# Optimization experiments

Hardware: AMD Instinct MI355X
Metric: run time of the kernel (lower is better)

The kernel has to match this reference:

```python
import jax, jax.numpy as jnp
import numpy as np

B, N, C, H = 8, 1025, 512, 8
G = 32  # grid size; S = G*G = N-1


def setup_inputs() -> dict:
    key = jax.random.key(0)
    ks = jax.random.split(key, 5)
    return {
        "x": jax.random.normal(ks[0], (B, N, C), dtype=jnp.float32),
        "qkv_w": jax.random.normal(ks[1], (3 * C, C), dtype=jnp.float32) * (C ** -0.5),
        "proj_w": jax.random.normal(ks[2], (C, C), dtype=jnp.float32) * (C ** -0.5),
        "proj_b": jnp.zeros((C,), dtype=jnp.float32),
        "wg_w": jax.random.normal(ks[3], (H, 64), dtype=jnp.float32) * 0.125,
        "wg_b": jnp.zeros((H,), dtype=jnp.float32),
    }


def _geometry_bias(wg_w, wg_b):
    # BoxRelationalEmbedding on a fixed 32x32 grid; batch-independent, so computed once.
    S = G * G
    xs = jnp.arange(G, dtype=jnp.float32)
    px = jnp.repeat(xs, G)   # px_min: row index per flattened cell
    py = jnp.tile(xs, G)     # py_min: col index per flattened cell
    rx0, ry0 = px / G, py / G
    rx1, ry1 = (px + 1.0) / G, (py + 1.0) / G
    cx = 0.5 * (rx0 + rx1)
    cy = 0.5 * (ry0 + ry1)
    w = rx1 - rx0 + 1.0
    h = ry1 - ry0 + 1.0
    dx = jnp.log(jnp.clip(jnp.abs((cx[:, None] - cx[None, :]) / w[:, None]), 1e-3, None))
    dy = jnp.log(jnp.clip(jnp.abs((cy[:, None] - cy[None, :]) / h[:, None]), 1e-3, None))
    dw = jnp.log(w[:, None] / w[None, :])
    dh = jnp.log(h[:, None] / h[None, :])
    pos = jnp.stack([dx, dy, dw, dh], axis=-1)  # [S,S,4]
    dim_mat = 1.0 / jnp.power(1000.0, jnp.arange(8, dtype=jnp.float32) / 8.0)  # dim_g/8 = 8 freqs
    mul = (100.0 * pos)[..., None] * dim_mat        # [S,S,4,8]
    mul = mul.reshape(S, S, 32)
    emb = jnp.concatenate([jnp.sin(mul), jnp.cos(mul)], axis=-1)  # [S,S,64]
    rgw = jax.nn.relu(jnp.einsum('ijd,hd->hij', emb, wg_w) + wg_b[:, None, None])  # [H,S,S]
    rgw = jnp.log(jnp.clip(rgw, 1e-6, None))
    # pad zero column (dim 3 cat of t1) then zero row (dim 2 cat of t2) -> [H, S+1, S+1]
    return jnp.pad(rgw, ((0, 0), (1, 0), (1, 0)))


def reference(x, qkv_w, proj_w, proj_b, wg_w, wg_b):
    b, n, c = x.shape
    hd = c // H
    scale = hd ** -0.5
    bias = _geometry_bias(wg_w, wg_b)  # [H, n, n]
    qkv = (x @ qkv_w.T).reshape(b, n, 3, H, hd)
    q, k, v = qkv[:, :, 0], qkv[:, :, 1], qkv[:, :, 2]  # each [b,n,H,hd]
    attn = jnp.einsum('bihd,bjhd->bhij', q, k) * scale + bias[None]
    attn = jax.nn.softmax(attn, axis=-1)
    out = jnp.einsum('bhij,bjhd->bihd', attn, v).reshape(b, n, c)
    return out @ proj_w.T + proj_b
```

## Files before the change

### kernel.cpp

```cpp
#include <hip/hip_runtime.h>
#include <hip/hip_bf16.h>
#include <math.h>

#define B_  8
#define N_  1025
#define C_  512
#define H_  8
#define HD_ 64
#define M_  (B_ * N_)
#define VCS 2048
#define VST 36

typedef __attribute__((ext_vector_type(8))) short short8;
typedef __attribute__((ext_vector_type(4))) float f32x4;

__device__ inline unsigned short bf16u(float x) {
    __hip_bfloat16 t = __float2bfloat16(x);
    return *(unsigned short*)&t;
}
__device__ inline void load_lds16(const void* g, void* l) {
    __builtin_amdgcn_global_load_lds(
        (const __attribute__((address_space(1))) unsigned int*)g,
        (__attribute__((address_space(3))) unsigned int*)l, 16, 0, 0);
}

#define PER_ ((size_t)B_ * H_ * N_ * HD_)
#define SZ_QKVW (3 * C_ * C_)
#define SZ_PRJW (C_ * C_)
#define CAST_BLKS ((4198400 + 786432 + 262144) / 4 / 256)

__global__ void prep_kernel(const float* __restrict__ x,
                            const float* __restrict__ qkv_w,
                            const float* __restrict__ proj_w,
                            const float* __restrict__ wg_w,
                            const float* __restrict__ wg_b,
                            unsigned short* __restrict__ xb,
                            unsigned short* __restrict__ wqkvb,
                            unsigned short* __restrict__ wprjb,
                            float* __restrict__ tab) {
    int blk = blockIdx.x;
    int tid = threadIdx.x;
    if (blk < 32) {
        int idx = blk * 256 + tid;
        int h = idx >> 10;
        int a = (idx >> 5) & 31;
        int b = idx & 31;
        float dx = logf(fmaxf((float)a * (1.0f / 33.0f), 0.001f));
        float dy = logf(fmaxf((float)b * (1.0f / 33.0f), 0.001f));
        const float* w = wg_w + h * 64;
        float acc = wg_b[h];
#pragma unroll
        for (int k = 0; k < 8; k++) {
            float f = powf(1000.0f, -(float)k * 0.125f);
            float X = 100.0f * dx * f;
            float Y = 100.0f * dy * f;
            acc += w[k]      * sinf(X);
            acc += w[8 + k]  * sinf(Y);
            acc += w[32 + k] * cosf(X);
            acc += w[40 + k] * cosf(Y);
            acc += w[48 + k] + w[56 + k];
        }
        tab[idx] = logf(fmaxf(fmaxf(acc, 0.0f), 1e-6f));
        return;
    }
    long i4 = ((long)(blk - 32) * 256 + tid) * 4;
    const float* src;
    unsigned short* dst;
    long off;
    if (i4 < (long)PER_)                    { src = x;      dst = xb;    off = i4; }
    else if (i4 < (long)PER_ + SZ_QKVW)     { src = qkv_w;  dst = wqkvb; off = i4 - PER_; }
    else                                    { src = proj_w; dst = wprjb; off = i4 - PER_ - SZ_QKVW; }
    float4 v = *(const float4*)(src + off);
    ushort4 p;
    p.x = bf16u(v.x); p.y = bf16u(v.y); p.z = bf16u(v.z); p.w = bf16u(v.w);
    *(ushort4*)(dst + off) = p;
}

#define GK 512

__global__ __launch_bounds__(256) void gemm_qkv_mfma(
        const unsigned short* __restrict__ A, const unsigned short* __restrict__ W,
        unsigned short* __restrict__ qb, unsigned short* __restrict__ kb,
        unsigned short* __restrict__ vtc) {
    __shared__ __align__(16) unsigned short As[128 * 32];
    __shared__ __align__(16) unsigned short Bs[128 * 32];
    int tid = threadIdx.x;
    int w = tid >> 6, lane = tid & 63;
    int quad = lane >> 4, l16 = lane & 15;
    int m0 = blockIdx.y * 128;
    int n0 = blockIdx.x * 128;
    int wr = (w >> 1) * 64, wc = (w & 1) * 64;

    int c0 = tid, c1 = tid + 256;
    int a_r0 = min(m0 + (c0 >> 2), M_ - 1), a_c0 = (c0 & 3) * 8;
    int a_r1 = min(m0 + (c1 >> 2), M_ - 1), a_c1 = (c1 & 3) * 8;
    int b_r0 = n0 + (c0 >> 2), b_r1 = n0 + (c1 >> 2);

    int which = n0 >> 9;
    int h = ((n0 + wc) >> 6) & 7;

    f32x4 acc[4][4];
    const f32x4 zero4 = {0.f, 0.f, 0.f, 0.f};
#pragma unroll
    for (int mi = 0; mi < 4; mi++)
#pragma unroll
        for (int ni = 0; ni < 4; ni++) acc[mi][ni] = zero4;

    for (int k0 = 0; k0 < GK; k0 += 32) {
        __syncthreads();
        load_lds16(A + (size_t)a_r0 * GK + k0 + a_c0, &As[w * 512]);
        load_lds16(A + (size_t)a_r1 * GK + k0 + a_c1, &As[2048 + w * 512]);
        load_lds16(W + (size_t)b_r0 * GK + k0 + a_c0, &Bs[w * 512]);
        load_lds16(W + (size_t)b_r1 * GK + k0 + a_c1, &Bs[2048 + w * 512]);
        __syncthreads();
        short8 af[4], bf[4];
#pragma unroll
        for (int mi = 0; mi < 4; mi++)
            af[mi] = *(const short8*)&As[(wr + mi * 16 + l16) * 32 + quad * 8];
#pragma unroll
        for (int ni = 0; ni < 4; ni++)
            bf[ni] = *(const short8*)&Bs[(wc + ni * 16 + l16) * 32 + quad * 8];
#pragma unroll
        for (int mi = 0; mi < 4; mi++)
#pragma unroll
            for (int ni = 0; ni < 4; ni++)
                acc[mi][ni] = __builtin_amdgcn_mfma_f32_16x16x32_bf16(
                    bf[ni], af[mi], acc[mi][ni], 0, 0, 0);
    }

    if (which < 2) {
        unsigned short* dst = (which == 0) ? qb : kb;
        float sc = (which == 0) ? 0.125f : 1.0f;
#pragma unroll
        for (int mi = 0; mi < 4; mi++) {
            int m = m0 + wr + mi * 16 + l16;
            if (m < M_) {
                int bb = m / N_;
                int i  = m - bb * N_;
                unsigned short* row = dst + ((size_t)(bb * H_ + h) * N_ + i) * HD_;
#pragma unroll
                for (int ni = 0; ni < 4; ni++) {
                    ushort4 pk;
                    pk.x = bf16u(acc[mi][ni][0] * sc);
                    pk.y = bf16u(acc[mi][ni][1] * sc);
                    pk.z = bf16u(acc[mi][ni][2] * sc);
                    pk.w = bf16u(acc[mi][ni][3] * sc);
                    *(ushort4*)(row + ni * 16 + quad * 4) = pk;
                }
            }
        }
    } else {
#pragma unroll
        for (int mi = 0; mi < 4; mi++) {
            int m = m0 + wr + mi * 16 + l16;
            if (m < M_) {
                int bb = m / N_;
                int i  = m - bb * N_;
                int ch = i >> 5, key = i & 31;
                unsigned short* base = vtc + ((size_t)(bb * H_ + h) * VST + ch) * VCS + key;
#pragma unroll
                for (int ni = 0; ni < 4; ni++)
#pragma unroll
                    for (int reg = 0; reg < 4; reg++)
                        base[(ni * 16 + quad * 4 + reg) * 32] = bf16u(acc[mi][ni][reg]);
            }
        }
    }
}

__global__ __launch_bounds__(256) void gemm_proj_mfma(
        const unsigned short* __restrict__ A, const unsigned short* __restrict__ W,
        const float* __restrict__ bias, float* __restrict__ out) {
    __shared__ __align__(16) unsigned short As[128 * 32];
    __shared__ __align__(16) unsigned short Bs[128 * 32];
    int tid = threadIdx.x;
    int w = tid >> 6, lane = tid & 63;
    int quad = lane >> 4, l16 = lane & 15;
    int m0 = blockIdx.y * 128;
    int n0 = blockIdx.x * 128;
    int wr = (w >> 1) * 64, wc = (w & 1) * 64;

    int c0 = tid, c1 = tid + 256;
    int a_r0 = min(m0 + (c0 >> 2), M_ - 1), a_c0 = (c0 & 3) * 8;
    int a_r1 = min(m0 + (c1 >> 2), M_ - 1), a_c1 = (c1 & 3) * 8;
    int b_r0 = n0 + (c0 >> 2), b_r1 = n0 + (c1 >> 2);

    f32x4 acc[4][4];
    const f32x4 zero4 = {0.f, 0.f, 0.f, 0.f};
#pragma unroll
    for (int mi = 0; mi < 4; mi++)
#pragma unroll
        for (int ni = 0; ni < 4; ni++) acc[mi][ni] = zero4;

    for (int k0 = 0; k0 < GK; k0 += 32) {
        __syncthreads();
        load_lds16(A + (size_t)a_r0 * GK + k0 + a_c0, &As[w * 512]);
        load_lds16(A + (size_t)a_r1 * GK + k0 + a_c1, &As[2048 + w * 512]);
        load_lds16(W + (size_t)b_r0 * GK + k0 + a_c0, &Bs[w * 512]);
        load_lds16(W + (size_t)b_r1 * GK + k0 + a_c1, &Bs[2048 + w * 512]);
        __syncthreads();
        short8 af[4], bf[4];
#pragma unroll
        for (int mi = 0; mi < 4; mi++)
            af[mi] = *(const short8*)&As[(wr + mi * 16 + l16) * 32 + quad * 8];
#pragma unroll
        for (int ni = 0; ni < 4; ni++)
            bf[ni] = *(const short8*)&Bs[(wc + ni * 16 + l16) * 32 + quad * 8];
#pragma unroll
        for (int mi = 0; mi < 4; mi++)
#pragma unroll
            for (int ni = 0; ni < 4; ni++)
                acc[mi][ni] = __builtin_amdgcn_mfma_f32_16x16x32_bf16(
                    af[mi], bf[ni], acc[mi][ni], 0, 0, 0);
    }

    float bvals[4];
#pragma unroll
    for (int ni = 0; ni < 4; ni++) bvals[ni] = bias[n0 + wc + ni * 16 + l16];
#pragma unroll
    for (int mi = 0; mi < 4; mi++)
#pragma unroll
        for (int reg = 0; reg < 4; reg++) {
            int m = m0 + wr + mi * 16 + quad * 4 + reg;
            if (m < M_) {
                float* row = out + (size_t)m * C_ + n0 + wc;
#pragma unroll
                for (int ni = 0; ni < 4; ni++)
                    row[ni * 16 + l16] = acc[mi][ni][reg] + bvals[ni];
            }
        }
}

#define RT_ 144

__global__ __launch_bounds__(576) void attn_fused(
        const unsigned short* __restrict__ qg,
        const unsigned short* __restrict__ kg,
        const unsigned short* __restrict__ vtc,
        const float* __restrict__ tab,
        unsigned short* __restrict__ ob) {
    __shared__ __align__(16) unsigned short Ks[2][6144];
    __shared__ __align__(16) unsigned short Vs[2][6144];
    __shared__ __align__(16) unsigned short Pw[9][16 * 40];
    __shared__ float tabs[1089];

    int tid = threadIdx.x;
    int w = tid >> 6, lane = tid & 63;
    int quad = lane >> 4, l16 = lane & 15;

    int lin = blockIdx.x;
    int xcd = lin & 7;
    int u = lin >> 3;
    int bhi = u & 7;
    int mt = u >> 3;
    int bh = xcd * 8 + bhi;
    int b = bh >> 3, h = bh & 7;

    const unsigned short* qp = qg + (size_t)bh * N_ * HD_;
    const unsigned short* kp = kg + (size_t)bh * N_ * HD_;
    const unsigned short* vp = vtc + (size_t)bh * VST * VCS;

    for (int i = tid; i < 1024; i += 576)
        tabs[(i >> 5) * 33 + (i & 31)] = tab[h * 1024 + i];

    short8 qf[2];
    {
        int row = min(mt * RT_ + w * 16 + l16, N_ - 1);
        qf[0] = *(const short8*)(qp + (size_t)row * HD_ + quad * 8);
        qf[1] = *(const short8*)(qp + (size_t)row * HD_ + 32 + quad * 8);
    }

    int rpx[4], rpy[4];
    bool rz[4];
#pragma unroll
    for (int reg = 0; reg < 4; reg++) {
        int r = mt * RT_ + w * 16 + quad * 4 + reg;
        int ri = min(max(r - 1, 0), N_ - 2);
        rpx[reg] = ri >> 5;
        rpy[reg] = ri & 31;
        rz[reg] = (r == 0);
    }

    f32x4 o_acc[4], l_acc;
    const f32x4 zero4 = {0.f, 0.f, 0.f, 0.f};
#pragma unroll
    for (int g2 = 0; g2 < 4; g2++) o_acc[g2] = zero4;
    l_acc = zero4;
    short8 ones;
    {
        short one_bf = (short)0x3F80;
#pragma unroll
        for (int j = 0; j < 8; j++) ones[j] = one_bf;
    }

    auto stage = [&](int t, int buf) {
        if (w < 6) {
#pragma unroll
            for (int r2 = 0; r2 < 2; r2++) {
                int cb = (r2 * 6 + w) * 64;
                int ch = cb + lane;
                int ct = ch >> 7, rem = ch & 127;
                int oct = rem >> 4, k16 = rem & 15;
                int key = min(t * 96 + ct * 16 + k16, N_ - 1);
                load_lds16(kp + (size_t)key * HD_ + oct * 8, &Ks[buf][cb * 8]);
            }
        } else {
            int wv = w - 6;
#pragma unroll
            for (int r2 = 0; r2 < 4; r2++) {
                int cb = (r2 * 3 + wv) * 64;
                load_lds16(vp + (size_t)t * 3 * VCS + (size_t)(cb + lane) * 8,
                           &Vs[buf][cb * 8]);
            }
        }
    };

    stage(0, 0);

#pragma unroll 1
    for (int t = 0; t < 11; t++) {
        int buf = t & 1;
        __syncthreads();
        if (t < 10) stage(t + 1, buf ^ 1);

        f32x4 s[6];
#pragma unroll
        for (int ct = 0; ct < 6; ct++) {
            short8 b0 = *(const short8*)&Ks[buf][(ct * 128 + quad * 16 + l16) * 8];
            short8 b1 = *(const short8*)&Ks[buf][(ct * 128 + (4 + quad) * 16 + l16) * 8];
            s[ct] = __builtin_amdgcn_mfma_f32_16x16x32_bf16(qf[0], b0, zero4, 0, 0, 0);
            s[ct] = __builtin_amdgcn_mfma_f32_16x16x32_bf16(qf[1], b1, s[ct], 0, 0, 0);
        }

#pragma unroll
        for (int ks = 0; ks < 3; ks++) {
#pragma unroll
            for (int ctl = 0; ctl < 2; ctl++) {
                int ct = ks * 2 + ctl;
                int col = t * 96 + ct * 16 + l16;
                int ji = col - 1;
                int cx = ji >> 5, cy = ji & 31;
                bool cz = (col == 0), co = (col >= N_);
#pragma unroll
                for (int reg = 0; reg < 4; reg++) {
                    float bia = 0.f;
                    if (!rz[reg] && !cz) {
                        int da = __sad(rpx[reg], cx, 0u);
                        int db = __sad(rpy[reg], cy, 0u);
                        bia = tabs[da * 33 + db];
                    }
                    float p = co ? 0.f : __expf(s[ct][reg] + bia);
                    Pw[w][(quad * 4 + reg) * 40 + ctl * 16 + l16] = bf16u(p);
                }
            }
            short8 pf = *(const short8*)&Pw[w][l16 * 40 + quad * 8];
            const unsigned short* vcp = &Vs[buf][ks * 2048 + quad * 8];
#pragma unroll
            for (int g2 = 0; g2 < 4; g2++) {
                short8 vf = *(const short8*)(vcp + (g2 * 16 + l16) * 32);
                o_acc[g2] = __builtin_amdgcn_mfma_f32_16x16x32_bf16(
                    pf, vf, o_acc[g2], 0, 0, 0);
            }
            l_acc = __builtin_amdgcn_mfma_f32_16x16x32_bf16(pf, ones, l_acc, 0, 0, 0);
        }
    }

#pragma unroll
    for (int reg = 0; reg < 4; reg++) {
        int r = mt * RT_ + w * 16 + quad * 4 + reg;
        if (r < N_) {
            float inv = 1.0f / l_acc[reg];
            unsigned short* orow = ob + ((size_t)b * N_ + r) * C_ + h * HD_ + l16;
#pragma unroll
            for (int g2 = 0; g2 < 4; g2++)
                orow[g2 * 16] = bf16u(o_acc[g2][reg] * inv);
        }
    }
}

extern "C" void kernel_launch(void* const* d_in, const int* in_sizes, int n_in,
                              void* d_out, int out_size, void* d_ws, size_t ws_size,
                              hipStream_t stream) {
    const float* x      = (const float*)d_in[0];
    const float* qkv_w  = (const float*)d_in[1];
    const float* proj_w = (const float*)d_in[2];
    const float* proj_b = (const float*)d_in[3];
    const float* wg_w   = (const float*)d_in[4];
    const float* wg_b   = (const float*)d_in[5];
    float* out = (float*)d_out;

    const size_t per = PER_;
    char* ws = (char*)d_ws;
    float* tab            = (float*)ws;
    unsigned short* xb    = (unsigned short*)(ws + (32 << 10));
    unsigned short* wqkvb = xb + per;
    unsigned short* wprjb = wqkvb + (size_t)SZ_QKVW;
    unsigned short* qb    = wprjb + (size_t)SZ_PRJW;
    unsigned short* kb    = qb + per;
    unsigned short* vtc   = kb + per;
    unsigned short* ob    = vtc + (size_t)64 * VST * VCS;

    prep_kernel<<<32 + CAST_BLKS, 256, 0, stream>>>(x, qkv_w, proj_w, wg_w, wg_b,
                                                    xb, wqkvb, wprjb, tab);
    gemm_qkv_mfma<<<dim3(12, 65), 256, 0, stream>>>(xb, wqkvb, qb, kb, vtc);
    attn_fused<<<8 * 8 * 8, 576, 0, stream>>>(qb, kb, vtc, tab, ob);
    gemm_proj_mfma<<<dim3(4, 65), 256, 0, stream>>>(ob, wprjb, proj_b, out);
}
```

Measured before the change: 198.6 us.

## Precompute dense fp16 bias table, switch softmax to exp2, pad V layout

```diff
diff --git a/kernel.cpp b/kernel.cpp
--- a/kernel.cpp
+++ b/kernel.cpp
@@ -1,5 +1,6 @@
 #include <hip/hip_runtime.h>
 #include <hip/hip_bf16.h>
+#include <hip/hip_fp16.h>
 #include <math.h>
 
 #define B_  8
@@ -8,7 +9,7 @@
 #define H_  8
 #define HD_ 64
 #define M_  (B_ * N_)
-#define VCS 2048
+#define VCS 2560
 #define VST 36
 
 typedef __attribute__((ext_vector_type(8))) short short8;
@@ -17,6 +18,11 @@
 __device__ inline unsigned short bf16u(float x) {
     __hip_bfloat16 t = __float2bfloat16(x);
     return *(unsigned short*)&t;
+}
+__device__ inline float fexp2(float x) {
+    float r;
+    asm("v_exp_f32 %0, %1" : "=v"(r) : "v"(x));
+    return r;
 }
 __device__ inline void load_lds16(const void* g, void* l) {
     __builtin_amdgcn_global_load_lds(
@@ -60,7 +66,7 @@
             acc += w[40 + k] * cosf(Y);
             acc += w[48 + k] + w[56 + k];
         }
-        tab[idx] = logf(fmaxf(fmaxf(acc, 0.0f), 1e-6f));
+        tab[idx] = log2f(fmaxf(fmaxf(acc, 0.0f), 1e-6f));
         return;
     }
     long i4 = ((long)(blk - 32) * 256 + tid) * 4;
@@ -74,6 +80,36 @@
     ushort4 p;
     p.x = bf16u(v.x); p.y = bf16u(v.y); p.z = bf16u(v.z); p.w = bf16u(v.w);
     *(ushort4*)(dst + off) = p;
+}
+
+__global__ __launch_bounds__(256) void bias_expand(const float* __restrict__ tab,
+                                                   unsigned short* __restrict__ big) {
+    int idx = blockIdx.x * 256 + threadIdx.x;
+    int cw = idx % 132;
+    int rh = idx / 132;
+    int r  = rh % 1152;
+    int h  = rh / 1152;
+    int c0 = cw * 8;
+    int i  = min(r, 1024) - 1;
+    int ix = i >> 5, iy = i & 31;
+    const float* th = tab + h * 1024;
+    unsigned short o8[8];
+#pragma unroll
+    for (int e = 0; e < 8; e++) {
+        int c = c0 + e;
+        float v;
+        if (r == 0 || c == 0) v = 0.f;
+        else if (c > 1024)    v = -60000.f;
+        else {
+            int j = c - 1;
+            int da = __sad(ix, j >> 5, 0u);
+            int db = __sad(iy, j & 31, 0u);
+            v = th[da * 32 + db];
+        }
+        __half hv = __float2half(v);
+        o8[e] = *(unsigned short*)&hv;
+    }
+    *(short8*)(big + (size_t)rh * 1056 + c0) = *(short8*)o8;
 }
 
 #define GK 512
@@ -130,7 +166,7 @@
 
     if (which < 2) {
         unsigned short* dst = (which == 0) ? qb : kb;
-        float sc = (which == 0) ? 0.125f : 1.0f;
+        float sc = (which == 0) ? 0.18033688f : 1.0f;
 #pragma unroll
         for (int mi = 0; mi < 4; mi++) {
             int m = m0 + wr + mi * 16 + l16;
@@ -157,12 +193,13 @@
                 int bb = m / N_;
                 int i  = m - bb * N_;
                 int ch = i >> 5, key = i & 31;
-                unsigned short* base = vtc + ((size_t)(bb * H_ + h) * VST + ch) * VCS + key;
+                int slot = ((key & 15) << 1) | (key >> 4);
+                unsigned short* base = vtc + ((size_t)(bb * H_ + h) * VST + ch) * VCS + slot;
 #pragma unroll
                 for (int ni = 0; ni < 4; ni++)
 #pragma unroll
                     for (int reg = 0; reg < 4; reg++)
-                        base[(ni * 16 + quad * 4 + reg) * 32] = bf16u(acc[mi][ni][reg]);
+                        base[(ni * 16 + quad * 4 + reg) * 40] = bf16u(acc[mi][ni][reg]);
             }
         }
     }
@@ -233,16 +270,15 @@
 
 #define RT_ 144
 
-__global__ __launch_bounds__(576) void attn_fused(
+__global__ __launch_bounds__(576, 5) void attn_fused(
         const unsigned short* __restrict__ qg,
         const unsigned short* __restrict__ kg,
         const unsigned short* __restrict__ vtc,
-        const float* __restrict__ tab,
+        const unsigned short* __restrict__ bigtab,
         unsigned short* __restrict__ ob) {
     __shared__ __align__(16) unsigned short Ks[2][6144];
-    __shared__ __align__(16) unsigned short Vs[2][6144];
-    __shared__ __align__(16) unsigned short Pw[9][16 * 40];
-    __shared__ float tabs[1089];
+    __shared__ __align__(16) unsigned short Vs[2][7680];
+    __shared__ __align__(16) unsigned short Pw[9][640];
 
     int tid = threadIdx.x;
     int w = tid >> 6, lane = tid & 63;
@@ -260,25 +296,14 @@
     const unsigned short* kp = kg + (size_t)bh * N_ * HD_;
     const unsigned short* vp = vtc + (size_t)bh * VST * VCS;
 
-    for (int i = tid; i < 1024; i += 576)
-        tabs[(i >> 5) * 33 + (i & 31)] = tab[h * 1024 + i];
+    int rbase = mt * RT_ + w * 16 + quad * 4;
+    const unsigned short* bt = bigtab + ((size_t)h * 1152 + rbase) * 1056 + l16;
 
     short8 qf[2];
     {
         int row = min(mt * RT_ + w * 16 + l16, N_ - 1);
         qf[0] = *(const short8*)(qp + (size_t)row * HD_ + quad * 8);
         qf[1] = *(const short8*)(qp + (size_t)row * HD_ + 32 + quad * 8);
-    }
-
-    int rpx[4], rpy[4];
-    bool rz[4];
-#pragma unroll
-    for (int reg = 0; reg < 4; reg++) {
-        int r = mt * RT_ + w * 16 + quad * 4 + reg;
-        int ri = min(max(r - 1, 0), N_ - 2);
-        rpx[reg] = ri >> 5;
-        rpy[reg] = ri & 31;
-        rz[reg] = (r == 0);
     }
 
     f32x4 o_acc[4], l_acc;
@@ -307,7 +332,7 @@
         } else {
             int wv = w - 6;
 #pragma unroll
-            for (int r2 = 0; r2 < 4; r2++) {
+            for (int r2 = 0; r2 < 5; r2++) {
                 int cb = (r2 * 3 + wv) * 64;
                 load_lds16(vp + (size_t)t * 3 * VCS + (size_t)(cb + lane) * 8,
                            &Vs[buf][cb * 8]);
@@ -321,43 +346,46 @@
     for (int t = 0; t < 11; t++) {
         int buf = t & 1;
         __syncthreads();
+
+        unsigned short blv[3][2][4];
+        const unsigned short* btp = bt + t * 96;
+#pragma unroll
+        for (int ks = 0; ks < 3; ks++)
+#pragma unroll
+            for (int ctl = 0; ctl < 2; ctl++)
+#pragma unroll
+                for (int reg = 0; reg < 4; reg++)
+                    blv[ks][ctl][reg] = btp[reg * 1056 + (ks * 2 + ctl) * 16];
+
         if (t < 10) stage(t + 1, buf ^ 1);
 
         f32x4 s[6];
 #pragma unroll
         for (int ct = 0; ct < 6; ct++) {
-            short8 b0 = *(const short8*)&Ks[buf][(ct * 128 + quad * 16 + l16) * 8];
-            short8 b1 = *(const short8*)&Ks[buf][(ct * 128 + (4 + quad) * 16 + l16) * 8];
-            s[ct] = __builtin_amdgcn_mfma_f32_16x16x32_bf16(qf[0], b0, zero4, 0, 0, 0);
-            s[ct] = __builtin_amdgcn_mfma_f32_16x16x32_bf16(qf[1], b1, s[ct], 0, 0, 0);
+            short8 kf0 = *(const short8*)&Ks[buf][(ct * 128 + quad * 16 + l16) * 8];
+            short8 kf1 = *(const short8*)&Ks[buf][(ct * 128 + (4 + quad) * 16 + l16) * 8];
+            s[ct] = __builtin_amdgcn_mfma_f32_16x16x32_bf16(qf[0], kf0, zero4, 0, 0, 0);
+            s[ct] = __builtin_amdgcn_mfma_f32_16x16x32_bf16(qf[1], kf1, s[ct], 0, 0, 0);
         }
 
 #pragma unroll
         for (int ks = 0; ks < 3; ks++) {
 #pragma unroll
-            for (int ctl = 0; ctl < 2; ctl++) {
-                int ct = ks * 2 + ctl;
-                int col = t * 96 + ct * 16 + l16;
-                int ji = col - 1;
-                int cx = ji >> 5, cy = ji & 31;
-                bool cz = (col == 0), co = (col >= N_);
-#pragma unroll
-                for (int reg = 0; reg < 4; reg++) {
-                    float bia = 0.f;
-                    if (!rz[reg] && !cz) {
-                        int da = __sad(rpx[reg], cx, 0u);
-                        int db = __sad(rpy[reg], cy, 0u);
-                        bia = tabs[da * 33 + db];
-                    }
-                    float p = co ? 0.f : __expf(s[ct][reg] + bia);
-                    Pw[w][(quad * 4 + reg) * 40 + ctl * 16 + l16] = bf16u(p);
-                }
+            for (int reg = 0; reg < 4; reg++) {
+                float bia0 = __half2float(*(const __half*)&blv[ks][0][reg]);
+                float bia1 = __half2float(*(const __half*)&blv[ks][1][reg]);
+                float p0 = fexp2(s[ks * 2][reg] + bia0);
+                float p1 = fexp2(s[ks * 2 + 1][reg] + bia1);
+                ushort2 pp;
+                pp.x = bf16u(p0);
+                pp.y = bf16u(p1);
+                *(ushort2*)&Pw[w][(quad * 4 + reg) * 40 + l16 * 2] = pp;
             }
             short8 pf = *(const short8*)&Pw[w][l16 * 40 + quad * 8];
-            const unsigned short* vcp = &Vs[buf][ks * 2048 + quad * 8];
+            const unsigned short* vcp = &Vs[buf][ks * 2560 + quad * 8];
 #pragma unroll
             for (int g2 = 0; g2 < 4; g2++) {
-                short8 vf = *(const short8*)(vcp + (g2 * 16 + l16) * 32);
+                short8 vf = *(const short8*)(vcp + (g2 * 16 + l16) * 40);
                 o_acc[g2] = __builtin_amdgcn_mfma_f32_16x16x32_bf16(
                     pf, vf, o_acc[g2], 0, 0, 0);
             }
@@ -367,7 +395,7 @@
 
 #pragma unroll
     for (int reg = 0; reg < 4; reg++) {
-        int r = mt * RT_ + w * 16 + quad * 4 + reg;
+        int r = rbase + reg;
         if (r < N_) {
             float inv = 1.0f / l_acc[reg];
             unsigned short* orow = ob + ((size_t)b * N_ + r) * C_ + h * HD_ + l16;
@@ -391,18 +419,20 @@
 
     const size_t per = PER_;
     char* ws = (char*)d_ws;
-    float* tab            = (float*)ws;
-    unsigned short* xb    = (unsigned short*)(ws + (32 << 10));
-    unsigned short* wqkvb = xb + per;
-    unsigned short* wprjb = wqkvb + (size_t)SZ_QKVW;
-    unsigned short* qb    = wprjb + (size_t)SZ_PRJW;
-    unsigned short* kb    = qb + per;
-    unsigned short* vtc   = kb + per;
-    unsigned short* ob    = vtc + (size_t)64 * VST * VCS;
+    float* tab             = (float*)ws;
+    unsigned short* bigtab = (unsigned short*)(ws + (32 << 10));
+    unsigned short* xb     = bigtab + (size_t)8 * 1152 * 1056;
+    unsigned short* wqkvb  = xb + per;
+    unsigned short* wprjb  = wqkvb + (size_t)SZ_QKVW;
+    unsigned short* qb     = wprjb + (size_t)SZ_PRJW;
+    unsigned short* kb     = qb + per;
+    unsigned short* vtc    = kb + per;
+    unsigned short* ob     = vtc + (size_t)64 * VST * VCS;
 
     prep_kernel<<<32 + CAST_BLKS, 256, 0, stream>>>(x, qkv_w, proj_w, wg_w, wg_b,
                                                     xb, wqkvb, wprjb, tab);
+    bias_expand<<<4752, 256, 0, stream>>>(tab, bigtab);
     gemm_qkv_mfma<<<dim3(12, 65), 256, 0, stream>>>(xb, wqkvb, qb, kb, vtc);
-    attn_fused<<<8 * 8 * 8, 576, 0, stream>>>(qb, kb, vtc, tab, ob);
+    attn_fused<<<8 * 8 * 8, 576, 0, stream>>>(qb, kb, vtc, bigtab, ob);
     gemm_proj_mfma<<<dim3(4, 65), 256, 0, stream>>>(ob, wprjb, proj_b, out);
 }
```

New measurement: 229.8 us. 1.16x slower.
